# Kernel optimization log

Hardware: AMD Instinct MI355X
Metric: run time of the kernel (lower is better)

The kernel has to match this reference:

```python
import jax, jax.numpy as jnp
import numpy as np

B, L, R, F = 16, 64, 256, 64
LIG_NIN, REC_NIN, EIN, EEMB = 32, 40, 16, 16
DEG = 8
E_LIG, E_REC = B * L * DEG, B * R * DEG
NL = 3
PNAMES = ["emb_nW", "emb_nb", "emb_eW", "emb_eb", "hidW", "hidb", "ln0_g", "ln0_b",
          "efW", "efb", "convb", "outW", "outb", "lng", "lnb"]
INT_NAMES = ("lig_src", "lig_dst", "rec_src", "rec_dst")


def _lrelu(v):
    return jax.nn.leaky_relu(v, 0.01)


def _ln(x, g, b):
    m = x.mean(-1, keepdims=True)
    v = ((x - m) ** 2).mean(-1, keepdims=True)
    return (x - m) / jnp.sqrt(v + 1e-5) * g + b


def _side(node_x, edge_x, src, dst, n_nodes, p):
    # GraphEmbedding: linear node/edge embedding
    eh = edge_x @ p["emb_eW"] + p["emb_eb"]                      # [E, EEMB]
    h = _lrelu(node_x @ p["emb_nW"] + p["emb_nb"]) @ p["hidW"] + p["hidb"]
    h = _ln(h, p["ln0_g"], p["ln0_b"])                           # [N, F]
    deg = jax.ops.segment_sum(jnp.ones(src.shape[0], jnp.float32), dst, num_segments=n_nodes)
    deg = jnp.maximum(deg, 1.0)[:, None]
    prev = []
    for i in range(NL):
        hh = _lrelu(h)
        # NNConv: per-edge F x F weight conditioned on edge features
        We = (eh @ p["efW"][i] + p["efb"][i]).reshape(-1, F, F)  # [E, F, F]
        msg = jnp.einsum('ei,eio->eo', hh[src], We)              # [E, F]
        agg = jax.ops.segment_sum(msg, dst, num_segments=n_nodes) / deg + p["convb"][i]
        h = _ln(_lrelu(agg) @ p["outW"][i] + p["outb"][i], p["lng"][i], p["lnb"][i])
        if i >= 2:  # residual to layer i-2
            h = h + prev[i - 2]
        prev.append(h)
    return h


def _forward(fl, lig_src, lig_dst, rec_src, rec_dst):
    lig_p = {n: fl["lig_" + n] for n in PNAMES}
    rec_p = {n: fl["rec_" + n] for n in PNAMES}
    lig_h = _side(fl["lig_x"], fl["lig_e"], lig_src, lig_dst, B * L, lig_p)
    rec_h = _side(fl["rec_x"], fl["rec_e"], rec_src, rec_dst, B * R, rec_p)
    # per-graph einsum('lf,rf->lr') scoring, batched since graphs are equal-sized
    op = jnp.einsum('blf,brf->blr', lig_h.reshape(B, L, F), rec_h.reshape(B, R, F))
    out = op.mean((1, 2))
    return out, op


def setup_inputs() -> dict:
    key = jax.random.key(0)
    it = iter(jax.random.split(key, 80))
    def nrm(shape, s=0.1):
        return jax.random.normal(next(it), shape, jnp.float32) * s
    inp = {}
    inp["lig_x"] = nrm((B * L, LIG_NIN), 1.0)
    inp["rec_x"] = nrm((B * R, REC_NIN), 1.0)
    inp["lig_e"] = nrm((E_LIG, EIN), 1.0)
    inp["rec_e"] = nrm((E_REC, EIN), 1.0)
    def edges(npg, epg, k1, k2):
        offs = (jnp.arange(B) * npg)[:, None]
        s = (jax.random.randint(k1, (B, epg), 0, npg) + offs).reshape(-1).astype(jnp.int32)
        d = (jax.random.randint(k2, (B, epg), 0, npg) + offs).reshape(-1).astype(jnp.int32)
        return s, d
    inp["lig_src"], inp["lig_dst"] = edges(L, L * DEG, next(it), next(it))
    inp["rec_src"], inp["rec_dst"] = edges(R, R * DEG, next(it), next(it))
    for pre, nin in (("lig", LIG_NIN), ("rec", REC_NIN)):
        inp[pre + "_emb_nW"] = nrm((nin, F)); inp[pre + "_emb_nb"] = nrm((F,))
        inp[pre + "_emb_eW"] = nrm((EIN, EEMB)); inp[pre + "_emb_eb"] = nrm((EEMB,))
        inp[pre + "_hidW"] = nrm((F, F)); inp[pre + "_hidb"] = nrm((F,))
        inp[pre + "_ln0_g"] = jnp.ones((F,)); inp[pre + "_ln0_b"] = jnp.zeros((F,))
        inp[pre + "_efW"] = nrm((NL, EEMB, F * F), 0.05); inp[pre + "_efb"] = nrm((NL, F * F), 0.05)
        inp[pre + "_convb"] = nrm((NL, F))
        inp[pre + "_outW"] = nrm((NL, F, F)); inp[pre + "_outb"] = nrm((NL, F))
        inp[pre + "_lng"] = jnp.ones((NL, F)); inp[pre + "_lnb"] = jnp.zeros((NL, F))
    return inp


def reference(lig_x, rec_x, lig_e, rec_e, lig_src, lig_dst, rec_src, rec_dst,
              lig_emb_nW, lig_emb_nb, lig_emb_eW, lig_emb_eb, lig_hidW, lig_hidb,
              lig_ln0_g, lig_ln0_b, lig_efW, lig_efb, lig_convb, lig_outW, lig_outb,
              lig_lng, lig_lnb,
              rec_emb_nW, rec_emb_nb, rec_emb_eW, rec_emb_eb, rec_hidW, rec_hidb,
              rec_ln0_g, rec_ln0_b, rec_efW, rec_efb, rec_convb, rec_outW, rec_outb,
              rec_lng, rec_lnb):
    all_args = dict(locals())
    fl = {k: v for k, v in all_args.items() if k not in INT_NAMES}
    return _forward(fl, lig_src, lig_dst, rec_src, rec_dst)
```

## Files before the change

### kernel.cpp

```cpp
#include <hip/hip_runtime.h>
#include <hip/hip_bf16.h>

#define NLIG 1024
#define NREC 4096
#define NTOT 5120
#define ELIG 8192
#define ETOT 40960
#define TPAD 1092

typedef __bf16 bf16x8 __attribute__((ext_vector_type(8)));
typedef float f32x4 __attribute__((ext_vector_type(4)));

struct Params {
  const float *lig_x, *rec_x, *lig_e, *rec_e;
  const int *lig_src, *lig_dst, *rec_src, *rec_dst;
  const float *nW[2], *nb[2], *eW[2], *eb[2], *hW[2], *hb[2], *g0[2], *b0[2];
  const float *efW[2], *efb[2], *convb[2], *outW[2], *outb[2], *lng[2], *lnb[2];
  float *aggA, *aggB, *prev0, *eh;
  __bf16 *Abf, *Wp, *oWp;
  int *deg;
  unsigned *bkt;
  int *bktbase, *bktcnt;
  float *out;
};

__device__ __forceinline__ float lrelu(float v){ return v > 0.f ? v : 0.01f * v; }

__device__ __forceinline__ float wsum(float v){
  #pragma unroll
  for (int off = 32; off > 0; off >>= 1) v += __shfl_xor(v, off, 64);
  return v;
}

__device__ __forceinline__ void window(int bid, int& side, int& r0, int& gr0,
                                       int& ebase, int& ecnt, int& egbase,
                                       const int*& srcArr, const int*& dstArr,
                                       const Params& p){
  if (bid < 64){
    side = 0; int b = bid >> 2, w = bid & 3;
    r0 = b*64 + w*16; gr0 = r0; ebase = b*512; ecnt = 512; egbase = ebase;
    srcArr = p.lig_src; dstArr = p.lig_dst;
  } else {
    side = 1; int g = bid - 64; int b = g >> 4, w = g & 15;
    r0 = b*256 + w*16; gr0 = NLIG + r0; ebase = b*2048; ecnt = 2048; egbase = ELIG + ebase;
    srcArr = p.rec_src; dstArr = p.rec_dst;
  }
}

__global__ __launch_bounds__(1024) void k_pre(Params p){
  __shared__ float sW[2][256], sb[2][16];
  __shared__ float nwl[40*64];
  __shared__ float hwl[64*64];
  __shared__ float sx[16][40], st[16][64];
  __shared__ int scnt[16], sbase[16], scur[16], dcnt[16];
  const int tid = threadIdx.x, bid = blockIdx.x;
  const int lane = tid & 63, wid = tid >> 6;
  const int gtid = bid*1024 + tid;

  int side, r0, gr0, ebase, ecnt, egbase;
  const int *srcArr, *dstArr;
  window(bid, side, r0, gr0, ebase, ecnt, egbase, srcArr, dstArr, p);
  const int nin = side ? 40 : 32;

  if (tid < 256){ sW[0][tid] = p.eW[0][tid]; sW[1][tid] = p.eW[1][tid]; }
  if (tid < 16){ sb[0][tid] = p.eb[0][tid]; sb[1][tid] = p.eb[1][tid];
                 scnt[tid] = 0; dcnt[tid] = 0; }
  for (int i = tid; i < nin*64; i += 1024) nwl[i] = p.nW[side][i];
  for (int i = tid; i < 4096; i += 1024) hwl[i] = p.hW[side][i];
  __syncthreads();

  if (gtid < 52224){
    int l  = gtid & 63;
    int t2 = gtid >> 6;
    int kk = t2 & 1;
    int t3 = t2 >> 1;
    int ct = t3 % 68;
    int sl = t3 / 68;
    int sd = sl / 3, ly = sl % 3;
    int ocol = ct*16 + (l & 15);
    int kslot = ocol >> 6, oo = ocol & 63;
    const float* src = (kslot < 16)
        ? (p.efW[sd] + (size_t)ly*16*4096 + (size_t)kslot*4096)
        : (p.efb[sd] + (size_t)ly*4096);
    bf16x8 w;
    #pragma unroll
    for (int j = 0; j < 8; j++){
      int i = kk*32 + (l >> 4)*8 + j;
      w[j] = (__bf16)src[i*64 + oo];
    }
    ((bf16x8*)p.Wp)[(size_t)sl*68*2*64 + (ct*2 + kk)*64 + l] = w;
  } else if (gtid < 52224 + 3072){
    int id2 = gtid - 52224;
    int l = id2 & 63;
    int t2 = id2 >> 6;
    int kk = t2 & 1;
    int ct = (t2 >> 1) & 3;
    int sl = t2 >> 3;
    int sd = sl / 3, ly = sl % 3;
    const float* src = p.outW[sd] + (size_t)ly*4096;
    bf16x8 w;
    #pragma unroll
    for (int j = 0; j < 8; j++){
      int i = kk*32 + (l >> 4)*8 + j;
      w[j] = (__bf16)src[i*64 + ct*16 + (l & 15)];
    }
    ((bf16x8*)p.oWp)[(size_t)(sl*8 + ct*2 + kk)*64 + l] = w;
  }

  if (gtid < ETOT){
    int e = gtid;
    int esd = e >= ELIG;
    int el = esd ? e - ELIG : e;
    const float* ex = (esd ? p.rec_e : p.lig_e) + (size_t)el * 16;
    float x[16];
    #pragma unroll
    for (int j = 0; j < 16; j += 4){
      float4 v = *(const float4*)(ex + j);
      x[j] = v.x; x[j+1] = v.y; x[j+2] = v.z; x[j+3] = v.w;
    }
    float s[16];
    #pragma unroll
    for (int k = 0; k < 16; k++){
      float acc = sb[esd][k];
      #pragma unroll
      for (int j = 0; j < 16; j++) acc += x[j] * sW[esd][j*16 + k];
      s[k] = acc;
    }
    float* ehp = p.eh + (size_t)e * 16;
    #pragma unroll
    for (int k = 0; k < 16; k += 4)
      *(float4*)(ehp + k) = make_float4(s[k], s[k+1], s[k+2], s[k+3]);
  }

  for (int i = gtid; i < NTOT*64; i += 320*1024){ p.aggA[i] = 0.f; p.aggB[i] = 0.f; }
  if (gtid < 16) p.out[gtid] = 0.f;

  {
    int n = gr0 + wid;
    int nl = r0 + wid;
    const float* x = (side ? p.rec_x : p.lig_x) + (size_t)nl * nin;
    if (lane < nin) sx[wid][lane] = x[lane];
    float tv = p.nb[side][lane];
    for (int j = 0; j < nin; j++) tv += sx[wid][j] * nwl[j*64 + lane];
    st[wid][lane] = lrelu(tv);
    float hv = p.hb[side][lane];
    #pragma unroll 8
    for (int j = 0; j < 64; j++) hv += st[wid][j] * hwl[j*64 + lane];
    float m = wsum(hv) * (1.f/64.f);
    float d = hv - m;
    float v = wsum(d*d) * (1.f/64.f);
    float o = d * rsqrtf(v + 1e-5f) * p.g0[side][lane] + p.b0[side][lane];
    p.Abf[(size_t)n*64 + lane] = (__bf16)lrelu(o);
  }

  for (int i = tid; i < ecnt; i += 1024){
    int s = srcArr[ebase + i];
    if ((unsigned)(s - r0) < 16u) atomicAdd(&scnt[s - r0], 1);
    int d = dstArr[ebase + i];
    if ((unsigned)(d - r0) < 16u) atomicAdd(&dcnt[d - r0], 1);
  }
  __syncthreads();
  if (tid < 64){
    int v = (lane < 16) ? scnt[lane] : 0;
    int pre = v;
    #pragma unroll
    for (int off = 1; off < 16; off <<= 1){
      int u = __shfl_up(pre, off, 64);
      if (lane >= off) pre += u;
    }
    if (lane < 16){ sbase[lane] = pre - v; scur[lane] = pre - v; }
  }
  if (tid < 16) p.deg[gr0 + tid] = dcnt[tid];
  __syncthreads();
  for (int i = tid; i < ecnt; i += 1024){
    int s = srcArr[ebase + i];
    if ((unsigned)(s - r0) < 16u){
      int d = dstArr[ebase + i];
      int pos = atomicAdd(&scur[s - r0], 1);
      p.bkt[(size_t)bid*2048 + pos] = ((unsigned)d << 16) | (unsigned)i;
    }
  }
  if (tid < 16){ p.bktbase[bid*16 + tid] = sbase[tid]; p.bktcnt[bid*16 + tid] = scnt[tid]; }
}

__global__ __launch_bounds__(1024, 8) void k_layer(Params p, int layer){
  const int tid = threadIdx.x, bid = blockIdx.x;
  const int lane = tid & 63, wid = tid >> 6;
  int side, r0, gr0, ebase, ecnt, egbase;
  const int *srcArr, *dstArr;
  window(bid, side, r0, gr0, ebase, ecnt, egbase, srcArr, dstArr, p);
  float* aggR = (layer == 1) ? p.aggA : p.aggB;
  float* aggW = (layer == 1) ? p.aggB : p.aggA;

  __shared__ __bf16 Tl[16][TPAD];
  __shared__ __bf16 albf[16][64];
  __shared__ __bf16 sabf[16][64];
  __shared__ float updo[16][68];

  if (layer > 0){
    int lm1 = layer - 1;
    int n = gr0 + wid;
    float a = aggR[(size_t)n*64 + lane];
    aggR[(size_t)n*64 + lane] = 0.f;
    float dg = fmaxf((float)p.deg[n], 1.f);
    a = lrelu(a / dg + p.convb[side][lm1*64 + lane]);
    sabf[wid][lane] = (__bf16)a;
    __syncthreads();
    if (wid < 4){
      int ct = wid;
      bf16x8 a0u, a1u;
      #pragma unroll
      for (int j = 0; j < 8; j++){
        a0u[j] = sabf[lane & 15][(lane >> 4)*8 + j];
        a1u[j] = sabf[lane & 15][32 + (lane >> 4)*8 + j];
      }
      const bf16x8* Ob = (const bf16x8*)p.oWp + (size_t)(side*3 + lm1)*8*64;
      bf16x8 b0 = Ob[(ct*2 + 0)*64 + lane];
      bf16x8 b1 = Ob[(ct*2 + 1)*64 + lane];
      f32x4 d = {0.f, 0.f, 0.f, 0.f};
      d = __builtin_amdgcn_mfma_f32_16x16x32_bf16(a0u, b0, d, 0, 0, 0);
      d = __builtin_amdgcn_mfma_f32_16x16x32_bf16(a1u, b1, d, 0, 0, 0);
      int orw = (lane >> 4)*4, ocl = ct*16 + (lane & 15);
      updo[orw+0][ocl] = d[0];
      updo[orw+1][ocl] = d[1];
      updo[orw+2][ocl] = d[2];
      updo[orw+3][ocl] = d[3];
    }
    __syncthreads();
    {
      float hv = p.outb[side][lm1*64 + lane] + updo[wid][lane];
      float m = wsum(hv) * (1.f/64.f);
      float d = hv - m;
      float v = wsum(d*d) * (1.f/64.f);
      float o = d * rsqrtf(v + 1e-5f) * p.lng[side][lm1*64 + lane] + p.lnb[side][lm1*64 + lane];
      if (layer == 1) p.prev0[(size_t)n*64 + lane] = o;
      albf[wid][lane] = (__bf16)lrelu(o);
    }
  }
  __syncthreads();

  bf16x8 a0, a1;
  if (layer == 0){
    const bf16x8* A = (const bf16x8*)(p.Abf + (size_t)(gr0 + (lane & 15))*64 + (lane >> 4)*8);
    a0 = A[0]; a1 = A[4];
  } else {
    #pragma unroll
    for (int j = 0; j < 8; j++){
      a0[j] = albf[lane & 15][(lane >> 4)*8 + j];
      a1[j] = albf[lane & 15][32 + (lane >> 4)*8 + j];
    }
  }
  const bf16x8* Wb = (const bf16x8*)p.Wp + (size_t)(side*3 + layer)*68*2*64;
  int orow = (lane >> 4)*4, ocol = lane & 15;
  {
    int ct = wid;
    bf16x8 b0 = Wb[(ct*2 + 0)*64 + lane];
    bf16x8 b1 = Wb[(ct*2 + 1)*64 + lane];
    while (ct < 68){
      int ctn = ct + 16;
      bf16x8 nb0 = b0, nb1 = b1;
      if (ctn < 68){ nb0 = Wb[(ctn*2 + 0)*64 + lane]; nb1 = Wb[(ctn*2 + 1)*64 + lane]; }
      f32x4 d = {0.f, 0.f, 0.f, 0.f};
      d = __builtin_amdgcn_mfma_f32_16x16x32_bf16(a0, b0, d, 0, 0, 0);
      d = __builtin_amdgcn_mfma_f32_16x16x32_bf16(a1, b1, d, 0, 0, 0);
      int col = ct*16 + ocol;
      Tl[orow+0][col] = (__bf16)d[0];
      Tl[orow+1][col] = (__bf16)d[1];
      Tl[orow+2][col] = (__bf16)d[2];
      Tl[orow+3][col] = (__bf16)d[3];
      b0 = nb0; b1 = nb1; ct = ctn;
    }
  }
  __syncthreads();

  {
    int cnt  = p.bktcnt[bid*16 + wid];
    if (cnt > 0){
      float t[17];
      #pragma unroll
      for (int k = 0; k < 17; k++) t[k] = (float)Tl[wid][k*64 + lane];
      size_t base = (size_t)bid*2048 + p.bktbase[bid*16 + wid];
      for (int c0 = 0; c0 < cnt; c0 += 64){
        int nn = min(64, cnt - c0);
        unsigned ew = (lane < nn) ? p.bkt[base + c0 + lane] : 0u;
        auto doe = [&](unsigned v){
          int gd = (int)(v >> 16) + (side ? NLIG : 0);
          int leid = (int)(v & 0xffffu);
          const float4* ehp = (const float4*)(p.eh + (size_t)(egbase + leid)*16);
          float4 v0 = ehp[0], v1 = ehp[1], v2 = ehp[2], v3 = ehp[3];
          float m = t[16];
          m += v0.x*t[0]  + v0.y*t[1]  + v0.z*t[2]  + v0.w*t[3];
          m += v1.x*t[4]  + v1.y*t[5]  + v1.z*t[6]  + v1.w*t[7];
          m += v2.x*t[8]  + v2.y*t[9]  + v2.z*t[10] + v2.w*t[11];
          m += v3.x*t[12] + v3.y*t[13] + v3.z*t[14] + v3.w*t[15];
          atomicAdd(&aggW[(size_t)gd*64 + lane], m);
        };
        int j = 0;
        for (; j + 2 <= nn; j += 2){
          unsigned e0 = __shfl(ew, j, 64), e1 = __shfl(ew, j+1, 64);
          doe(e0); doe(e1);
        }
        if (j < nn) doe(__shfl(ew, j, 64));
      }
    }
  }
}

__global__ __launch_bounds__(1024) void k_final(Params p){
  const int tid = threadIdx.x, bid = blockIdx.x;
  const int lane = tid & 63, wid = tid >> 6;
  int b = bid >> 4, rt = bid & 15;
  __shared__ float slh[64][65];
  __shared__ float srh[16][65];
  __shared__ float owl[2][4096];
  __shared__ float sa[16][64];
  __shared__ float ps[16];

  for (int idx = tid; idx < 4096; idx += 1024){
    owl[0][idx] = p.outW[0][2*4096 + idx];
    owl[1][idx] = p.outW[1][2*4096 + idx];
  }
  __syncthreads();

  for (int rr = wid; rr < 80; rr += 16){
    int side = rr >= 64;
    int n = side ? (NLIG + b*256 + rt*16 + (rr - 64)) : (b*64 + rr);
    float a = p.aggA[(size_t)n*64 + lane];
    float dg = fmaxf((float)p.deg[n], 1.f);
    a = lrelu(a / dg + p.convb[side][128 + lane]);
    sa[wid][lane] = a;
    float hv = p.outb[side][128 + lane];
    const float* ow = &owl[side][0];
    #pragma unroll 8
    for (int j = 0; j < 64; j++) hv += sa[wid][j] * ow[j*64 + lane];
    float m = wsum(hv) * (1.f/64.f);
    float d = hv - m;
    float v = wsum(d*d) * (1.f/64.f);
    float o = d * rsqrtf(v + 1e-5f) * p.lng[side][128 + lane] + p.lnb[side][128 + lane];
    o += p.prev0[(size_t)n*64 + lane];
    if (side) srh[rr - 64][lane] = o; else slh[rr][lane] = o;
  }
  __syncthreads();

  int r = tid & 15, lg = tid >> 4;
  float acc = 0.f;
  #pragma unroll 8
  for (int f = 0; f < 64; f++) acc += slh[lg][f] * srh[r][f];
  p.out[16 + (size_t)b*16384 + (size_t)lg*256 + rt*16 + r] = acc;

  float psum = wsum(acc);
  if (lane == 0) ps[wid] = psum;
  __syncthreads();
  if (tid == 0){
    float s = 0.f;
    #pragma unroll
    for (int i = 0; i < 16; i++) s += ps[i];
    atomicAdd(&p.out[b], s * (1.f/16384.f));
  }
}

extern "C" void kernel_launch(void* const* d_in, const int* in_sizes, int n_in,
                              void* d_out, int out_size, void* d_ws, size_t ws_size,
                              hipStream_t stream){
  Params p;
  p.lig_x  = (const float*)d_in[0];
  p.rec_x  = (const float*)d_in[1];
  p.lig_e  = (const float*)d_in[2];
  p.rec_e  = (const float*)d_in[3];
  p.lig_src = (const int*)d_in[4];
  p.lig_dst = (const int*)d_in[5];
  p.rec_src = (const int*)d_in[6];
  p.rec_dst = (const int*)d_in[7];
  for (int s = 0; s < 2; s++){
    const int o = 8 + s*15;
    p.nW[s]   = (const float*)d_in[o+0];  p.nb[s]   = (const float*)d_in[o+1];
    p.eW[s]   = (const float*)d_in[o+2];  p.eb[s]   = (const float*)d_in[o+3];
    p.hW[s]   = (const float*)d_in[o+4];  p.hb[s]   = (const float*)d_in[o+5];
    p.g0[s]   = (const float*)d_in[o+6];  p.b0[s]   = (const float*)d_in[o+7];
    p.efW[s]  = (const float*)d_in[o+8];  p.efb[s]  = (const float*)d_in[o+9];
    p.convb[s]= (const float*)d_in[o+10]; p.outW[s] = (const float*)d_in[o+11];
    p.outb[s] = (const float*)d_in[o+12]; p.lng[s]  = (const float*)d_in[o+13];
    p.lnb[s]  = (const float*)d_in[o+14];
  }
  char* W = (char*)d_ws;
  p.aggA  = (float*)W;  W += (size_t)NTOT*64*4;
  p.aggB  = (float*)W;  W += (size_t)NTOT*64*4;
  p.prev0 = (float*)W;  W += (size_t)NTOT*64*4;
  p.eh    = (float*)W;  W += (size_t)ETOT*16*4;
  p.Abf   = (__bf16*)W; W += (size_t)NTOT*64*2;
  p.Wp    = (__bf16*)W; W += (size_t)2*3*68*2*64*8*2;
  p.oWp   = (__bf16*)W; W += (size_t)2*3*4*2*64*8*2;
  p.deg   = (int*)W;    W += (size_t)NTOT*4;
  p.bkt   = (unsigned*)W; W += (size_t)320*2048*4;
  p.bktbase = (int*)W;  W += (size_t)320*16*4;
  p.bktcnt  = (int*)W;  W += (size_t)320*16*4;
  p.out   = (float*)d_out;

  k_pre<<<320, 1024, 0, stream>>>(p);
  k_layer<<<320, 1024, 0, stream>>>(p, 0);
  k_layer<<<320, 1024, 0, stream>>>(p, 1);
  k_layer<<<320, 1024, 0, stream>>>(p, 2);
  k_final<<<256, 1024, 0, stream>>>(p);
}
```

Measured before the change: 104.7 us.

## Replace atomic scatter aggregation with per-edge message buffers and dst-bucket gather; fuse layer0 into pre

Messages are now written per edge into a dense buffer, and each destination node gathers its incoming messages through a new dst-bucket list instead of using float atomicAdd into node aggregates. This removes the atomics and the zeroing of the aggregate buffers. The pre-kernel is fused with layer 0: node embedding, edge embedding for the block's source edges, the MFMA weight generation and the message computation all run in one launch, cutting one kernel launch. The cost is larger workspace traffic (E×64 message buffers written and re-read) and weight conversion done on the fly inside the fused kernel.

```diff
diff --git a/kernel.cpp b/kernel.cpp
--- a/kernel.cpp
+++ b/kernel.cpp
@@ -16,11 +16,10 @@
   const int *lig_src, *lig_dst, *rec_src, *rec_dst;
   const float *nW[2], *nb[2], *eW[2], *eb[2], *hW[2], *hb[2], *g0[2], *b0[2];
   const float *efW[2], *efb[2], *convb[2], *outW[2], *outb[2], *lng[2], *lnb[2];
-  float *aggA, *aggB, *prev0, *eh;
-  __bf16 *Abf, *Wp, *oWp;
-  int *deg;
-  unsigned *bkt;
-  int *bktbase, *bktcnt;
+  float *msgvA, *msgvB, *prev0, *eh;
+  __bf16 *Wp, *oWp;
+  unsigned short *sbkt, *dbkt;
+  int *sbg, *scg, *dbg, *dcg;
   float *out;
 };
 
@@ -47,12 +46,18 @@
   }
 }
 
-__global__ __launch_bounds__(1024) void k_pre(Params p){
-  __shared__ float sW[2][256], sb[2][16];
-  __shared__ float nwl[40*64];
-  __shared__ float hwl[64*64];
-  __shared__ float sx[16][40], st[16][64];
-  __shared__ int scnt[16], sbase[16], scur[16], dcnt[16];
+__global__ __launch_bounds__(1024, 8) void k_front(Params p){
+  union EmbT {
+    struct { float nwl[40*64], hwl[64*64], sx[16][40], st[16][64]; } e;
+    __bf16 Tl[16][TPAD];
+  };
+  __shared__ EmbT su;
+  __shared__ float sW[256], sb[16];
+  __shared__ __bf16 albf[16][64];
+  __shared__ unsigned short slist[2048];
+  __shared__ int scnt[16], sbase[16], scur[16], dcnt[16], dbase[16], dcur[16];
+  __shared__ int sTot;
+
   const int tid = threadIdx.x, bid = blockIdx.x;
   const int lane = tid & 63, wid = tid >> 6;
   const int gtid = bid*1024 + tid;
@@ -62,12 +67,11 @@
   window(bid, side, r0, gr0, ebase, ecnt, egbase, srcArr, dstArr, p);
   const int nin = side ? 40 : 32;
 
-  if (tid < 256){ sW[0][tid] = p.eW[0][tid]; sW[1][tid] = p.eW[1][tid]; }
-  if (tid < 16){ sb[0][tid] = p.eb[0][tid]; sb[1][tid] = p.eb[1][tid];
-                 scnt[tid] = 0; dcnt[tid] = 0; }
-  for (int i = tid; i < nin*64; i += 1024) nwl[i] = p.nW[side][i];
-  for (int i = tid; i < 4096; i += 1024) hwl[i] = p.hW[side][i];
-  __syncthreads();
+  if (tid < 256) sW[tid] = p.eW[side][tid];
+  if (tid < 16){ sb[tid] = p.eb[side][tid]; scnt[tid] = 0; dcnt[tid] = 0; }
+  for (int i = tid; i < nin*64; i += 1024) su.e.nwl[i] = p.nW[side][i];
+  for (int i = tid; i < 4096; i += 1024) su.e.hwl[i] = p.hW[side][i];
+  if (gtid < 16) p.out[gtid] = 0.f;
 
   if (gtid < 52224){
     int l  = gtid & 63;
@@ -106,52 +110,7 @@
     }
     ((bf16x8*)p.oWp)[(size_t)(sl*8 + ct*2 + kk)*64 + l] = w;
   }
-
-  if (gtid < ETOT){
-    int e = gtid;
-    int esd = e >= ELIG;
-    int el = esd ? e - ELIG : e;
-    const float* ex = (esd ? p.rec_e : p.lig_e) + (size_t)el * 16;
-    float x[16];
-    #pragma unroll
-    for (int j = 0; j < 16; j += 4){
-      float4 v = *(const float4*)(ex + j);
-      x[j] = v.x; x[j+1] = v.y; x[j+2] = v.z; x[j+3] = v.w;
-    }
-    float s[16];
-    #pragma unroll
-    for (int k = 0; k < 16; k++){
-      float acc = sb[esd][k];
-      #pragma unroll
-      for (int j = 0; j < 16; j++) acc += x[j] * sW[esd][j*16 + k];
-      s[k] = acc;
-    }
-    float* ehp = p.eh + (size_t)e * 16;
-    #pragma unroll
-    for (int k = 0; k < 16; k += 4)
-      *(float4*)(ehp + k) = make_float4(s[k], s[k+1], s[k+2], s[k+3]);
-  }
-
-  for (int i = gtid; i < NTOT*64; i += 320*1024){ p.aggA[i] = 0.f; p.aggB[i] = 0.f; }
-  if (gtid < 16) p.out[gtid] = 0.f;
-
-  {
-    int n = gr0 + wid;
-    int nl = r0 + wid;
-    const float* x = (side ? p.rec_x : p.lig_x) + (size_t)nl * nin;
-    if (lane < nin) sx[wid][lane] = x[lane];
-    float tv = p.nb[side][lane];
-    for (int j = 0; j < nin; j++) tv += sx[wid][j] * nwl[j*64 + lane];
-    st[wid][lane] = lrelu(tv);
-    float hv = p.hb[side][lane];
-    #pragma unroll 8
-    for (int j = 0; j < 64; j++) hv += st[wid][j] * hwl[j*64 + lane];
-    float m = wsum(hv) * (1.f/64.f);
-    float d = hv - m;
-    float v = wsum(d*d) * (1.f/64.f);
-    float o = d * rsqrtf(v + 1e-5f) * p.g0[side][lane] + p.b0[side][lane];
-    p.Abf[(size_t)n*64 + lane] = (__bf16)lrelu(o);
-  }
+  __syncthreads();
 
   for (int i = tid; i < ecnt; i += 1024){
     int s = srcArr[ebase + i];
@@ -169,41 +128,172 @@
       if (lane >= off) pre += u;
     }
     if (lane < 16){ sbase[lane] = pre - v; scur[lane] = pre - v; }
-  }
-  if (tid < 16) p.deg[gr0 + tid] = dcnt[tid];
+    if (lane == 15) sTot = pre;
+  } else if (tid < 128){
+    int v = (lane < 16) ? dcnt[lane] : 0;
+    int pre = v;
+    #pragma unroll
+    for (int off = 1; off < 16; off <<= 1){
+      int u = __shfl_up(pre, off, 64);
+      if (lane >= off) pre += u;
+    }
+    if (lane < 16){ dbase[lane] = pre - v; dcur[lane] = pre - v; }
+  }
   __syncthreads();
   for (int i = tid; i < ecnt; i += 1024){
     int s = srcArr[ebase + i];
     if ((unsigned)(s - r0) < 16u){
-      int d = dstArr[ebase + i];
       int pos = atomicAdd(&scur[s - r0], 1);
-      p.bkt[(size_t)bid*2048 + pos] = ((unsigned)d << 16) | (unsigned)i;
-    }
-  }
-  if (tid < 16){ p.bktbase[bid*16 + tid] = sbase[tid]; p.bktcnt[bid*16 + tid] = scnt[tid]; }
-}
-
-__global__ __launch_bounds__(1024, 8) void k_layer(Params p, int layer){
+      slist[pos] = (unsigned short)i;
+      p.sbkt[(size_t)bid*2048 + pos] = (unsigned short)i;
+    }
+    int d = dstArr[ebase + i];
+    if ((unsigned)(d - r0) < 16u){
+      int pos = atomicAdd(&dcur[d - r0], 1);
+      p.dbkt[(size_t)bid*2048 + pos] = (unsigned short)i;
+    }
+  }
+  if (tid < 16){
+    p.sbg[bid*16 + tid] = sbase[tid]; p.scg[bid*16 + tid] = scnt[tid];
+    p.dbg[bid*16 + tid] = dbase[tid]; p.dcg[bid*16 + tid] = dcnt[tid];
+  }
+
+  {
+    int nl = r0 + wid;
+    const float* x = (side ? p.rec_x : p.lig_x) + (size_t)nl * nin;
+    if (lane < nin) su.e.sx[wid][lane] = x[lane];
+    float tv = p.nb[side][lane];
+    for (int j = 0; j < nin; j++) tv += su.e.sx[wid][j] * su.e.nwl[j*64 + lane];
+    su.e.st[wid][lane] = lrelu(tv);
+    float hv = p.hb[side][lane];
+    #pragma unroll 8
+    for (int j = 0; j < 64; j++) hv += su.e.st[wid][j] * su.e.hwl[j*64 + lane];
+    float m = wsum(hv) * (1.f/64.f);
+    float d = hv - m;
+    float v = wsum(d*d) * (1.f/64.f);
+    float o = d * rsqrtf(v + 1e-5f) * p.g0[side][lane] + p.b0[side][lane];
+    albf[wid][lane] = (__bf16)lrelu(o);
+  }
+  __syncthreads();
+
+  {
+    int total = sTot;
+    const float* exb = side ? p.rec_e : p.lig_e;
+    for (int t2 = tid; t2 < total; t2 += 1024){
+      int el = slist[t2];
+      const float* ex = exb + (size_t)(ebase + el) * 16;
+      float x[16];
+      #pragma unroll
+      for (int j = 0; j < 16; j += 4){
+        float4 v = *(const float4*)(ex + j);
+        x[j] = v.x; x[j+1] = v.y; x[j+2] = v.z; x[j+3] = v.w;
+      }
+      float s[16];
+      #pragma unroll
+      for (int k = 0; k < 16; k++){
+        float acc = sb[k];
+        #pragma unroll
+        for (int j = 0; j < 16; j++) acc += x[j] * sW[j*16 + k];
+        s[k] = acc;
+      }
+      float* ehp = p.eh + (size_t)(egbase + el) * 16;
+      #pragma unroll
+      for (int k = 0; k < 16; k += 4)
+        *(float4*)(ehp + k) = make_float4(s[k], s[k+1], s[k+2], s[k+3]);
+    }
+  }
+  __threadfence_block();
+  __syncthreads();
+
+  {
+    bf16x8 a0, a1;
+    #pragma unroll
+    for (int j = 0; j < 8; j++){
+      a0[j] = albf[lane & 15][(lane >> 4)*8 + j];
+      a1[j] = albf[lane & 15][32 + (lane >> 4)*8 + j];
+    }
+    const float* W0 = p.efW[side];
+    const float* B0 = p.efb[side];
+    int orow = (lane >> 4)*4, ocol = lane & 15;
+    for (int ct = wid; ct < 68; ct += 16){
+      int oc = ct*16 + ocol;
+      int kslot = oc >> 6, oo = oc & 63;
+      const float* src = (kslot < 16) ? (W0 + (size_t)kslot*4096) : B0;
+      bf16x8 b0, b1;
+      #pragma unroll
+      for (int j = 0; j < 8; j++){
+        int i0 = (lane >> 4)*8 + j;
+        b0[j] = (__bf16)src[(size_t)i0*64 + oo];
+        b1[j] = (__bf16)src[(size_t)(32 + i0)*64 + oo];
+      }
+      f32x4 d = {0.f, 0.f, 0.f, 0.f};
+      d = __builtin_amdgcn_mfma_f32_16x16x32_bf16(a0, b0, d, 0, 0, 0);
+      d = __builtin_amdgcn_mfma_f32_16x16x32_bf16(a1, b1, d, 0, 0, 0);
+      int col = ct*16 + ocol;
+      su.Tl[orow+0][col] = (__bf16)d[0];
+      su.Tl[orow+1][col] = (__bf16)d[1];
+      su.Tl[orow+2][col] = (__bf16)d[2];
+      su.Tl[orow+3][col] = (__bf16)d[3];
+    }
+  }
+  __syncthreads();
+
+  {
+    int cnt = scnt[wid];
+    if (cnt > 0){
+      float t[17];
+      #pragma unroll
+      for (int k = 0; k < 17; k++) t[k] = (float)su.Tl[wid][k*64 + lane];
+      int base = sbase[wid];
+      auto doe = [&](int el){
+        const float4* ehp = (const float4*)(p.eh + (size_t)(egbase + el)*16);
+        float4 v0 = ehp[0], v1 = ehp[1], v2 = ehp[2], v3 = ehp[3];
+        float m = t[16];
+        m += v0.x*t[0]  + v0.y*t[1]  + v0.z*t[2]  + v0.w*t[3];
+        m += v1.x*t[4]  + v1.y*t[5]  + v1.z*t[6]  + v1.w*t[7];
+        m += v2.x*t[8]  + v2.y*t[9]  + v2.z*t[10] + v2.w*t[11];
+        m += v3.x*t[12] + v3.y*t[13] + v3.z*t[14] + v3.w*t[15];
+        p.msgvA[(size_t)(egbase + el)*64 + lane] = m;
+      };
+      int i = 0;
+      for (; i + 2 <= cnt; i += 2){ doe(slist[base+i]); doe(slist[base+i+1]); }
+      if (i < cnt) doe(slist[base+i]);
+    }
+  }
+}
+
+__global__ __launch_bounds__(1024, 8) void k_mid(Params p, int layer){
   const int tid = threadIdx.x, bid = blockIdx.x;
   const int lane = tid & 63, wid = tid >> 6;
   int side, r0, gr0, ebase, ecnt, egbase;
   const int *srcArr, *dstArr;
   window(bid, side, r0, gr0, ebase, ecnt, egbase, srcArr, dstArr, p);
-  float* aggR = (layer == 1) ? p.aggA : p.aggB;
-  float* aggW = (layer == 1) ? p.aggB : p.aggA;
+  const float* mi = (layer == 1) ? p.msgvA : p.msgvB;
+  float*       mo = (layer == 1) ? p.msgvB : p.msgvA;
 
   __shared__ __bf16 Tl[16][TPAD];
   __shared__ __bf16 albf[16][64];
   __shared__ __bf16 sabf[16][64];
   __shared__ float updo[16][68];
 
-  if (layer > 0){
+  {
     int lm1 = layer - 1;
-    int n = gr0 + wid;
-    float a = aggR[(size_t)n*64 + lane];
-    aggR[(size_t)n*64 + lane] = 0.f;
-    float dg = fmaxf((float)p.deg[n], 1.f);
-    a = lrelu(a / dg + p.convb[side][lm1*64 + lane]);
+    int cnt  = p.dcg[bid*16 + wid];
+    int base = p.dbg[bid*16 + wid];
+    const unsigned short* dl = p.dbkt + (size_t)bid*2048 + base;
+    float acc = 0.f;
+    int i = 0;
+    for (; i + 4 <= cnt; i += 4){
+      int e0 = dl[i], e1 = dl[i+1], e2 = dl[i+2], e3 = dl[i+3];
+      float x0 = mi[(size_t)(egbase + e0)*64 + lane];
+      float x1 = mi[(size_t)(egbase + e1)*64 + lane];
+      float x2 = mi[(size_t)(egbase + e2)*64 + lane];
+      float x3 = mi[(size_t)(egbase + e3)*64 + lane];
+      acc += (x0 + x1) + (x2 + x3);
+    }
+    for (; i < cnt; i++) acc += mi[(size_t)(egbase + dl[i])*64 + lane];
+    float dg = fmaxf((float)cnt, 1.f);
+    float a = lrelu(acc / dg + p.convb[side][lm1*64 + lane]);
     sabf[wid][lane] = (__bf16)a;
     __syncthreads();
     if (wid < 4){
@@ -233,26 +323,21 @@
       float d = hv - m;
       float v = wsum(d*d) * (1.f/64.f);
       float o = d * rsqrtf(v + 1e-5f) * p.lng[side][lm1*64 + lane] + p.lnb[side][lm1*64 + lane];
-      if (layer == 1) p.prev0[(size_t)n*64 + lane] = o;
+      if (layer == 1) p.prev0[(size_t)(gr0 + wid)*64 + lane] = o;
       albf[wid][lane] = (__bf16)lrelu(o);
     }
   }
   __syncthreads();
 
-  bf16x8 a0, a1;
-  if (layer == 0){
-    const bf16x8* A = (const bf16x8*)(p.Abf + (size_t)(gr0 + (lane & 15))*64 + (lane >> 4)*8);
-    a0 = A[0]; a1 = A[4];
-  } else {
+  {
+    bf16x8 a0, a1;
     #pragma unroll
     for (int j = 0; j < 8; j++){
       a0[j] = albf[lane & 15][(lane >> 4)*8 + j];
       a1[j] = albf[lane & 15][32 + (lane >> 4)*8 + j];
     }
-  }
-  const bf16x8* Wb = (const bf16x8*)p.Wp + (size_t)(side*3 + layer)*68*2*64;
-  int orow = (lane >> 4)*4, ocol = lane & 15;
-  {
+    const bf16x8* Wb = (const bf16x8*)p.Wp + (size_t)(side*3 + layer)*68*2*64;
+    int orow = (lane >> 4)*4, ocol = lane & 15;
     int ct = wid;
     bf16x8 b0 = Wb[(ct*2 + 0)*64 + lane];
     bf16x8 b1 = Wb[(ct*2 + 1)*64 + lane];
@@ -274,39 +359,30 @@
   __syncthreads();
 
   {
-    int cnt  = p.bktcnt[bid*16 + wid];
+    int cnt  = p.scg[bid*16 + wid];
     if (cnt > 0){
       float t[17];
       #pragma unroll
       for (int k = 0; k < 17; k++) t[k] = (float)Tl[wid][k*64 + lane];
-      size_t base = (size_t)bid*2048 + p.bktbase[bid*16 + wid];
-      for (int c0 = 0; c0 < cnt; c0 += 64){
-        int nn = min(64, cnt - c0);
-        unsigned ew = (lane < nn) ? p.bkt[base + c0 + lane] : 0u;
-        auto doe = [&](unsigned v){
-          int gd = (int)(v >> 16) + (side ? NLIG : 0);
-          int leid = (int)(v & 0xffffu);
-          const float4* ehp = (const float4*)(p.eh + (size_t)(egbase + leid)*16);
-          float4 v0 = ehp[0], v1 = ehp[1], v2 = ehp[2], v3 = ehp[3];
-          float m = t[16];
-          m += v0.x*t[0]  + v0.y*t[1]  + v0.z*t[2]  + v0.w*t[3];
-          m += v1.x*t[4]  + v1.y*t[5]  + v1.z*t[6]  + v1.w*t[7];
-          m += v2.x*t[8]  + v2.y*t[9]  + v2.z*t[10] + v2.w*t[11];
-          m += v3.x*t[12] + v3.y*t[13] + v3.z*t[14] + v3.w*t[15];
-          atomicAdd(&aggW[(size_t)gd*64 + lane], m);
-        };
-        int j = 0;
-        for (; j + 2 <= nn; j += 2){
-          unsigned e0 = __shfl(ew, j, 64), e1 = __shfl(ew, j+1, 64);
-          doe(e0); doe(e1);
-        }
-        if (j < nn) doe(__shfl(ew, j, 64));
-      }
-    }
-  }
-}
-
-__global__ __launch_bounds__(1024) void k_final(Params p){
+      const unsigned short* sl = p.sbkt + (size_t)bid*2048 + p.sbg[bid*16 + wid];
+      auto doe = [&](int el){
+        const float4* ehp = (const float4*)(p.eh + (size_t)(egbase + el)*16);
+        float4 v0 = ehp[0], v1 = ehp[1], v2 = ehp[2], v3 = ehp[3];
+        float m = t[16];
+        m += v0.x*t[0]  + v0.y*t[1]  + v0.z*t[2]  + v0.w*t[3];
+        m += v1.x*t[4]  + v1.y*t[5]  + v1.z*t[6]  + v1.w*t[7];
+        m += v2.x*t[8]  + v2.y*t[9]  + v2.z*t[10] + v2.w*t[11];
+        m += v3.x*t[12] + v3.y*t[13] + v3.z*t[14] + v3.w*t[15];
+        mo[(size_t)(egbase + el)*64 + lane] = m;
+      };
+      int i = 0;
+      for (; i + 2 <= cnt; i += 2){ doe(sl[i]); doe(sl[i+1]); }
+      if (i < cnt) doe(sl[i]);
+    }
+  }
+}
+
+__global__ __launch_bounds__(1024) void k_back(Params p){
   const int tid = threadIdx.x, bid = blockIdx.x;
   const int lane = tid & 63, wid = tid >> 6;
   int b = bid >> 4, rt = bid & 15;
@@ -324,10 +400,25 @@
 
   for (int rr = wid; rr < 80; rr += 16){
     int side = rr >= 64;
-    int n = side ? (NLIG + b*256 + rt*16 + (rr - 64)) : (b*64 + rr);
-    float a = p.aggA[(size_t)n*64 + lane];
-    float dg = fmaxf((float)p.deg[n], 1.f);
-    a = lrelu(a / dg + p.convb[side][128 + lane]);
+    int n, wbid, loc, egb;
+    if (!side){ n = b*64 + rr;                      wbid = b*4 + (rr >> 4); loc = rr & 15;  egb = b*512; }
+    else      { n = NLIG + b*256 + rt*16 + (rr-64); wbid = 64 + b*16 + rt;  loc = rr - 64;  egb = ELIG + b*2048; }
+    int cnt  = p.dcg[wbid*16 + loc];
+    int base = p.dbg[wbid*16 + loc];
+    const unsigned short* dl = p.dbkt + (size_t)wbid*2048 + base;
+    float acc = 0.f;
+    int i = 0;
+    for (; i + 4 <= cnt; i += 4){
+      int e0 = dl[i], e1 = dl[i+1], e2 = dl[i+2], e3 = dl[i+3];
+      float x0 = p.msgvA[(size_t)(egb + e0)*64 + lane];
+      float x1 = p.msgvA[(size_t)(egb + e1)*64 + lane];
+      float x2 = p.msgvA[(size_t)(egb + e2)*64 + lane];
+      float x3 = p.msgvA[(size_t)(egb + e3)*64 + lane];
+      acc += (x0 + x1) + (x2 + x3);
+    }
+    for (; i < cnt; i++) acc += p.msgvA[(size_t)(egb + dl[i])*64 + lane];
+    float dg = fmaxf((float)cnt, 1.f);
+    float a = lrelu(acc / dg + p.convb[side][128 + lane]);
     sa[wid][lane] = a;
     float hv = p.outb[side][128 + lane];
     const float* ow = &owl[side][0];
@@ -383,22 +474,22 @@
     p.lnb[s]  = (const float*)d_in[o+14];
   }
   char* W = (char*)d_ws;
-  p.aggA  = (float*)W;  W += (size_t)NTOT*64*4;
-  p.aggB  = (float*)W;  W += (size_t)NTOT*64*4;
+  p.msgvA = (float*)W;  W += (size_t)ETOT*64*4;
+  p.msgvB = (float*)W;  W += (size_t)ETOT*64*4;
   p.prev0 = (float*)W;  W += (size_t)NTOT*64*4;
   p.eh    = (float*)W;  W += (size_t)ETOT*16*4;
-  p.Abf   = (__bf16*)W; W += (size_t)NTOT*64*2;
   p.Wp    = (__bf16*)W; W += (size_t)2*3*68*2*64*8*2;
   p.oWp   = (__bf16*)W; W += (size_t)2*3*4*2*64*8*2;
-  p.deg   = (int*)W;    W += (size_t)NTOT*4;
-  p.bkt   = (unsigned*)W; W += (size_t)320*2048*4;
-  p.bktbase = (int*)W;  W += (size_t)320*16*4;
-  p.bktcnt  = (int*)W;  W += (size_t)320*16*4;
+  p.sbg   = (int*)W;    W += (size_t)320*16*4;
+  p.scg   = (int*)W;    W += (size_t)320*16*4;
+  p.dbg   = (int*)W;    W += (size_t)320*16*4;
+  p.dcg   = (int*)W;    W += (size_t)320*16*4;
+  p.sbkt  = (unsigned short*)W; W += (size_t)320*2048*2;
+  p.dbkt  = (unsigned short*)W; W += (size_t)320*2048*2;
   p.out   = (float*)d_out;
 
-  k_pre<<<320, 1024, 0, stream>>>(p);
-  k_layer<<<320, 1024, 0, stream>>>(p, 0);
-  k_layer<<<320, 1024, 0, stream>>>(p, 1);
-  k_layer<<<320, 1024, 0, stream>>>(p, 2);
-  k_final<<<256, 1024, 0, stream>>>(p);
-}
+  k_front<<<320, 1024, 0, stream>>>(p);
+  k_mid<<<320, 1024, 0, stream>>>(p, 1);
+  k_mid<<<320, 1024, 0, stream>>>(p, 2);
+  k_back<<<256, 1024, 0, stream>>>(p);
+}
```

Result: slower. 133.1 us (+27.1%).
